# Optimization experiments

Hardware: AMD Instinct MI355X
Metric: run time of the kernel (lower is better)

The kernel has to match this reference:

```python
import jax, jax.numpy as jnp
import numpy as np

D_MODEL = 1024
N_HEADS = 16
D_HEAD = D_MODEL // N_HEADS
SCALE = 1.0 / (D_HEAD ** 0.5)


def _rel_shift(t):
    # Transformer-XL relative shift: pad -> view -> slice -> view. t: [b,h,q,k]
    b, h, q, k = t.shape
    padded = jnp.pad(t, ((0, 0), (0, 0), (0, 0), (1, 0)))  # [b,h,q,k+1]
    shifted = padded.reshape(b, h, k + 1, q)[:, :, 1:, :].reshape(b, h, q, k)
    return shifted


def setup_inputs() -> dict:
    key = jax.random.key(0)
    ks = jax.random.split(key, 10)
    B, T, M = 2, 1024, 1024
    J = M + T
    inp = {
        "x": jax.random.normal(ks[0], (B, T, D_MODEL), dtype=jnp.float32),
        "memory": jax.random.normal(ks[1], (B, M, D_MODEL), dtype=jnp.float32),
        "pos_emb": jax.random.normal(ks[2], (J, D_MODEL), dtype=jnp.float32),
        # nn.Linear(d, d, bias=False) weights: y = x @ W.T, W: [out, in]
        "q_w": jax.random.normal(ks[3], (D_MODEL, D_MODEL), dtype=jnp.float32) * 0.02,
        "k_w": jax.random.normal(ks[4], (D_MODEL, D_MODEL), dtype=jnp.float32) * 0.02,
        "v_w": jax.random.normal(ks[5], (D_MODEL, D_MODEL), dtype=jnp.float32) * 0.02,
        "r_w": jax.random.normal(ks[6], (D_MODEL, D_MODEL), dtype=jnp.float32) * 0.02,
        "out_w": jax.random.normal(ks[7], (D_MODEL, D_MODEL), dtype=jnp.float32) * 0.02,
        "pos_bias_u": jax.random.normal(ks[8], (N_HEADS, D_HEAD), dtype=jnp.float32) * 0.02,
        "pos_bias_v": jax.random.normal(ks[9], (N_HEADS, D_HEAD), dtype=jnp.float32) * 0.02,
    }
    return inp


def reference(x, memory, pos_emb, q_w, k_w, v_w, r_w, out_w, pos_bias_u, pos_bias_v):
    B, T, _ = x.shape
    cat = jnp.concatenate([memory, x], axis=1)  # [B, M+T, d]
    L = cat.shape[1]

    def heads(t):  # [B, time, d] -> [B, h, time, dh]
        return t.reshape(t.shape[0], t.shape[1], N_HEADS, D_HEAD).transpose(0, 2, 1, 3)

    q = heads(x @ q_w.T)      # [B,h,T,dh]
    k = heads(cat @ k_w.T)    # [B,h,L,dh]
    v = heads(cat @ v_w.T)    # [B,h,L,dh]
    r = (pos_emb @ r_w.T).reshape(-1, N_HEADS, D_HEAD).transpose(1, 0, 2)  # [h,J,dh]

    q_u = q + pos_bias_u[None, :, None, :]
    q_v = q + pos_bias_v[None, :, None, :]

    content_score = jnp.einsum('bhqd,bhkd->bhqk', q_u, k)  # [B,h,T,L]
    rel_score = jnp.einsum('bhqd,hjd->bhqj', q_v, r)        # [B,h,T,J]
    rel_score = _rel_shift(rel_score)

    scores = (content_score + rel_score) * SCALE
    attn = jax.nn.softmax(scores, axis=-1)
    out = jnp.einsum('bhqk,bhkd->bhqd', attn, v)            # [B,h,T,dh]
    out = out.transpose(0, 2, 1, 3).reshape(B, T, N_HEADS * D_HEAD)
    return out @ out_w.T
```

## Files before the change

kernel.cpp:

```cpp
#include <hip/hip_runtime.h>


typedef unsigned short u16;
typedef unsigned int u32;
typedef short bf16x8 __attribute__((ext_vector_type(8)));
typedef float f32x4 __attribute__((ext_vector_type(4)));

#define MFMA16(a, b, c) __builtin_amdgcn_mfma_f32_16x16x32_bf16(a, b, c, 0, 0, 0)

__device__ __forceinline__ u16 f2bf(float f) {
  u32 u = __float_as_uint(f);
  u32 r = (u + 0x7fffu + ((u >> 16) & 1u)) >> 16;
  return (u16)r;
}

__device__ __forceinline__ void async16(void* lds, const void* g) {
  __builtin_amdgcn_global_load_lds(
      (const __attribute__((address_space(1))) u32*)g,
      (__attribute__((address_space(3))) u32*)lds, 16, 0, 0);
}

__global__ void prep_kernel(const float* __restrict__ x, const float* __restrict__ mem,
                            const float* __restrict__ pos,
                            const float* __restrict__ qw, const float* __restrict__ kw,
                            const float* __restrict__ vw, const float* __restrict__ rw,
                            const float* __restrict__ ow,
                            u16* __restrict__ catb, u16* __restrict__ posb,
                            u16* __restrict__ wqb, u16* __restrict__ wkb,
                            u16* __restrict__ wvb, u16* __restrict__ wrb,
                            u16* __restrict__ wob) {
  const int seg = blockIdx.y;
  const int vid = blockIdx.x * blockDim.x + threadIdx.x;
  const float* src = nullptr;
  u16* dst = nullptr;
  int count = 0;
  switch (seg) {
    case 0: count = (2 * 2048 * 1024) / 4; dst = catb; break;
    case 1: count = (2048 * 1024) / 4; src = pos; dst = posb; break;
    case 2: count = (1024 * 1024) / 4; src = qw; dst = wqb; break;
    case 3: count = (1024 * 1024) / 4; src = kw; dst = wkb; break;
    case 4: count = (1024 * 1024) / 4; src = vw; dst = wvb; break;
    case 5: count = (1024 * 1024) / 4; src = rw; dst = wrb; break;
    case 6: count = (1024 * 1024) / 4; src = ow; dst = wob; break;
  }
  if (vid >= count) return;
  float4 f;
  if (seg == 0) {
    int e = vid * 4;
    int col = e & 1023;
    int row = (e >> 10) & 2047;
    int b = e >> 21;
    const float* s2 = (row < 1024)
                          ? (mem + ((size_t)(b * 1024 + row) * 1024 + col))
                          : (x + ((size_t)(b * 1024 + (row - 1024)) * 1024 + col));
    f = *(const float4*)s2;
  } else {
    f = *(const float4*)(src + (size_t)vid * 4);
  }
  ushort4 o4;
  o4.x = f2bf(f.x); o4.y = f2bf(f.y); o4.z = f2bf(f.z); o4.w = f2bf(f.w);
  *(ushort4*)(dst + (size_t)vid * 4) = o4;
}

__device__ __forceinline__ void gemm_core(const u16* __restrict__ A, const u16* __restrict__ W,
                                          u16* As, u16* Bs, int m0, int n0, bool qmap,
                                          f32x4 acc[4][4]) {
  const int t = threadIdx.x;
  const int lane = t & 63, wid = t >> 6;
  const int colL = lane & 15, rg = lane >> 4;
  const int wm = (wid >> 1) * 64, wn = (wid & 1) * 64;
  for (int kt = 0; kt < 32; ++kt) {
    __syncthreads();
#pragma unroll
    for (int pass = 0; pass < 2; ++pass) {
      int slot = t + pass * 256;
      int row = slot >> 2, ch = slot & 3;
      int sch = ch ^ ((row >> 1) & 3);
      int ar = m0 + row;
      if (qmap) ar = ((ar >> 10) << 11) + 1024 + (ar & 1023);
      async16(As + slot * 8, A + (size_t)ar * 1024 + kt * 32 + sch * 8);
      async16(Bs + slot * 8, W + (size_t)(n0 + row) * 1024 + kt * 32 + sch * 8);
    }
    __syncthreads();
    bf16x8 af[4], bfr[4];
#pragma unroll
    for (int mi = 0; mi < 4; ++mi) {
      int r = wm + mi * 16 + colL;
      af[mi] = *(const bf16x8*)(As + r * 32 + (rg ^ ((r >> 1) & 3)) * 8);
    }
#pragma unroll
    for (int ni = 0; ni < 4; ++ni) {
      int r = wn + ni * 16 + colL;
      bfr[ni] = *(const bf16x8*)(Bs + r * 32 + (rg ^ ((r >> 1) & 3)) * 8);
    }
#pragma unroll
    for (int mi = 0; mi < 4; ++mi)
#pragma unroll
      for (int ni = 0; ni < 4; ++ni)
        acc[mi][ni] = MFMA16(af[mi], bfr[ni], acc[mi][ni]);
  }
}

__global__ __launch_bounds__(256, 2) void gemm_qkvr(
    const u16* __restrict__ catb, const u16* __restrict__ posb,
    const u16* __restrict__ wqb, const u16* __restrict__ wrb,
    const u16* __restrict__ wkb, const u16* __restrict__ wvb,
    const float* __restrict__ bu, const float* __restrict__ bv,
    u16* __restrict__ qub, u16* __restrict__ qvb, u16* __restrict__ rbuf,
    u16* __restrict__ kbuf, u16* __restrict__ vtbuf) {
  __shared__ u16 As[128 * 32], Bs[128 * 32];
  const int x = blockIdx.x;
  const int bid = (x & 7) * 96 + (x >> 3);
  const u16* A;
  const u16* W;
  int mode, r2;
  bool qmap = false;
  if (bid < 128)      { mode = 0; A = catb; W = wqb; qmap = true; r2 = bid; }
  else if (bid < 256) { mode = 1; A = posb; W = wrb; r2 = bid - 128; }
  else if (bid < 512) { mode = 2; A = catb; W = wkb; r2 = bid - 256; }
  else                { mode = 3; A = catb; W = wvb; r2 = bid - 512; }
  const int m0 = (r2 >> 3) * 128, n0 = (r2 & 7) * 128;
  f32x4 acc[4][4];
  f32x4 zz = {0.f, 0.f, 0.f, 0.f};
#pragma unroll
  for (int a1 = 0; a1 < 4; ++a1)
#pragma unroll
    for (int a2 = 0; a2 < 4; ++a2) acc[a1][a2] = zz;
  gemm_core(A, W, As, Bs, m0, n0, qmap, acc);
  const int t = threadIdx.x, lane = t & 63, wid = t >> 6;
  const int colL = lane & 15, rg = lane >> 4;
  const int wm = (wid >> 1) * 64, wn = (wid & 1) * 64;
  const float sc = 0.18033688f;
#pragma unroll
  for (int mi = 0; mi < 4; ++mi)
#pragma unroll
    for (int ni = 0; ni < 4; ++ni)
#pragma unroll
      for (int e = 0; e < 4; ++e) {
        int m = m0 + wm + mi * 16 + rg * 4 + e;
        int n = n0 + wn + ni * 16 + colL;
        float val = acc[mi][ni][e];
        int hh = n >> 6, dd = n & 63;
        if (mode == 0) {
          int bb = m >> 10, tq = m & 1023;
          size_t ad = (((size_t)(bb * 16 + hh)) * 1024 + tq) * 64 + dd;
          qub[ad] = f2bf((val + bu[n]) * sc);
          qvb[ad] = f2bf((val + bv[n]) * sc);
        } else if (mode == 1) {
          rbuf[((((size_t)hh * 128 + (m >> 4)) * 8 + (dd >> 3)) * 16 + (m & 15)) * 8 +
               (dd & 7)] = f2bf(val);
        } else {
          int bb = m >> 11, j = m & 2047;
          size_t bh2 = (size_t)(bb * 16 + hh);
          if (mode == 2)
            kbuf[(((bh2 * 128 + (j >> 4)) * 8 + (dd >> 3)) * 16 + (j & 15)) * 8 + (dd & 7)] =
                f2bf(val);
          else
            vtbuf[((((bh2 * 32 + (j >> 6)) * 4 + (dd >> 4)) * 8 + ((j >> 3) & 7)) * 16 +
                   (dd & 15)) * 8 + (j & 7)] = f2bf(val);
        }
      }
}

__global__ __launch_bounds__(256, 2) void attn_kernel(
    const u16* __restrict__ qu, const u16* __restrict__ qv, const u16* __restrict__ ktile,
    const u16* __restrict__ vtile, const u16* __restrict__ rtile,
    float* __restrict__ opart, float* __restrict__ mlpart) {
  __shared__ float Ulds[4][3200];
  const int t = threadIdx.x;
  const int wid = t >> 6, lane = t & 63;
  const int colL = lane & 15, rg = lane >> 4;
  const int bid = ((blockIdx.x & 7) << 6) | (blockIdx.x >> 3);
  const int bh = bid >> 4;
  const int rem = bid & 15;
  const int qc = rem >> 1, ks = rem & 1;
  const int h = bh & 15;
  const int i0 = qc * 128 + wid * 32;

  const u16* qub = qu + (size_t)bh * (1024 * 64);
  const u16* qvb = qv + (size_t)bh * (1024 * 64);
  const u16* kb = ktile + (size_t)bh * (128 * 1024);
  const u16* vb = vtile + (size_t)bh * (32 * 4096);
  const u16* rb = rtile + (size_t)h * (128 * 1024);
  const int lane8 = (rg * 16 + colL) * 8;

  bf16x8 aqu0[2], aqv0[2], aqu1[2], aqv1[2];
  {
    int r0 = i0 + colL;
    int r1 = i0 + 16 + colL;
#pragma unroll
    for (int kx = 0; kx < 2; ++kx) {
      aqu0[kx] = *(const bf16x8*)(qub + (size_t)r0 * 64 + kx * 32 + rg * 8);
      aqv0[kx] = *(const bf16x8*)(qvb + (size_t)r0 * 64 + kx * 32 + rg * 8);
      aqu1[kx] = *(const bf16x8*)(qub + (size_t)r1 * 64 + kx * 32 + rg * 8);
      aqv1[kx] = *(const bf16x8*)(qvb + (size_t)r1 * 64 + kx * 32 + rg * 8);
    }
  }
  bf16x8 ones;
#pragma unroll
  for (int i = 0; i < 8; ++i) ones[i] = (short)0x3F80;

  const f32x4 zz = {0.f, 0.f, 0.f, 0.f};
  f32x4 o0[4], o1[4];
  f32x4 lacc0 = zz, lacc1 = zz;
#pragma unroll
  for (int e = 0; e < 4; ++e) { o0[e] = zz; o1[e] = zz; }
  int lb0[4], lb1[4];
#pragma unroll
  for (int e = 0; e < 4; ++e) {
    lb0[e] = (rg * 4 + e) * 99 + colL + 31;
    lb1[e] = (rg * 4 + e) * 99 + colL + 1615;
  }

  float* Uw = &Ulds[wid][0];
  u16* Pw = (u16*)Uw;

#pragma unroll 1
  for (int jt = ks * 16; jt < ks * 16 + 16; ++jt) {
    const int j0 = jt * 64;
    f32x4 s0[4], s1[4];
#pragma unroll
    for (int ni = 0; ni < 4; ++ni) {
      const u16* kp = kb + (size_t)((j0 >> 4) + ni) * 1024 + lane8;
      bf16x8 b0 = *(const bf16x8*)kp;
      bf16x8 b1 = *(const bf16x8*)(kp + 512);
      s0[ni] = zz;
      s0[ni] = MFMA16(aqu0[0], b0, s0[ni]);
      s0[ni] = MFMA16(aqu0[1], b1, s0[ni]);
      s1[ni] = zz;
      s1[ni] = MFMA16(aqu1[0], b0, s1[ni]);
      s1[ni] = MFMA16(aqu1[1], b1, s1[ni]);
    }
    const int pbase2 = j0 + 992 - i0;
    const bool mainv = (pbase2 <= 2047);
    const bool leak = (pbase2 + 94 >= 2049);
    if (mainv) {
      const int tb = pbase2 >> 4;
      bf16x8 rc[12];
#pragma unroll
      for (int uc = 0; uc < 6; ++uc) {
        int tt = tb + uc;
        tt = tt < 127 ? tt : 127;
        const u16* rp = rb + (size_t)tt * 1024 + lane8;
        rc[2 * uc] = *(const bf16x8*)rp;
        rc[2 * uc + 1] = *(const bf16x8*)(rp + 512);
      }
#pragma unroll
      for (int uc = 1; uc < 6; ++uc) {
        f32x4 ua = zz;
        ua = MFMA16(aqv0[0], rc[2 * uc], ua);
        ua = MFMA16(aqv0[1], rc[2 * uc + 1], ua);
#pragma unroll
        for (int e = 0; e < 4; ++e) Uw[(rg * 4 + e) * 100 + uc * 16 + colL] = ua[e];
      }
#pragma unroll
      for (int uc = 0; uc < 5; ++uc) {
        f32x4 ub = zz;
        ub = MFMA16(aqv1[0], rc[2 * uc], ub);
        ub = MFMA16(aqv1[1], rc[2 * uc + 1], ub);
#pragma unroll
        for (int e = 0; e < 4; ++e) Uw[(16 + rg * 4 + e) * 100 + uc * 16 + colL] = ub[e];
      }
      asm volatile("s_waitcnt lgkmcnt(0)" ::: "memory");
      const int pl0 = pbase2 + colL + 31;
      const int pl1 = pbase2 + colL + 15;
#pragma unroll
      for (int c = 0; c < 4; ++c)
#pragma unroll
        for (int e = 0; e < 4; ++e) {
          int w0e = rg * 4 + e;
          float u0 = Uw[lb0[e] + c * 16];
          float u1 = Uw[lb1[e] + c * 16];
          int p0 = pl0 + c * 16 - w0e;
          int p1 = pl1 + c * 16 - w0e;
          s0[c][e] += (p0 <= 2047) ? u0 : 0.f;
          s1[c][e] += (p1 <= 2047) ? u1 : 0.f;
        }
    }
    if (leak) {
      asm volatile("s_waitcnt lgkmcnt(0)" ::: "memory");
      bf16x8 aqs0[2], aqs1[2];
      {
        int rs0 = i0 + colL + 1;
        int rs1 = i0 + 16 + colL + 1;
        rs1 = rs1 < 1024 ? rs1 : 1023;
#pragma unroll
        for (int kx = 0; kx < 2; ++kx) {
          aqs0[kx] = *(const bf16x8*)(qvb + (size_t)rs0 * 64 + kx * 32 + rg * 8);
          aqs1[kx] = *(const bf16x8*)(qvb + (size_t)rs1 * 64 + kx * 32 + rg * 8);
        }
      }
      const int mB1 = (pbase2 - 2048) >> 4;
      const int rowL = (colL + 15) & 15;
      const int tadj = (colL > 0) ? 0 : -1;
      bf16x8 r2[12];
#pragma unroll
      for (int uc = 0; uc < 6; ++uc) {
        int tL = mB1 + uc + tadj;
        tL = tL < 0 ? 0 : (tL > 127 ? 127 : tL);
        const u16* rp = rb + (size_t)tL * 1024 + rg * 128 + rowL * 8;
        r2[2 * uc] = *(const bf16x8*)rp;
        r2[2 * uc + 1] = *(const bf16x8*)(rp + 512);
      }
#pragma unroll
      for (int uc = 1; uc < 6; ++uc) {
        f32x4 ua = zz;
        ua = MFMA16(aqs0[0], r2[2 * uc], ua);
        ua = MFMA16(aqs0[1], r2[2 * uc + 1], ua);
#pragma unroll
        for (int e = 0; e < 4; ++e) Uw[(rg * 4 + e) * 100 + uc * 16 + colL] = ua[e];
      }
#pragma unroll
      for (int uc = 0; uc < 5; ++uc) {
        f32x4 ub = zz;
        ub = MFMA16(aqs1[0], r2[2 * uc], ub);
        ub = MFMA16(aqs1[1], r2[2 * uc + 1], ub);
#pragma unroll
        for (int e = 0; e < 4; ++e) Uw[(16 + rg * 4 + e) * 100 + uc * 16 + colL] = ub[e];
      }
      asm volatile("s_waitcnt lgkmcnt(0)" ::: "memory");
      const int pl0 = pbase2 + colL + 31;
      const int pl1 = pbase2 + colL + 15;
#pragma unroll
      for (int c = 0; c < 4; ++c)
#pragma unroll
        for (int e = 0; e < 4; ++e) {
          int w0e = rg * 4 + e;
          int p0 = pl0 + c * 16 - w0e;
          int p1 = pl1 + c * 16 - w0e;
          if (p0 >= 2049) s0[c][e] += Uw[lb0[e] + c * 16];
          if (p1 >= 2049) s1[c][e] += Uw[lb1[e] + c * 16];
        }
    }
    bf16x8 vf[8];
    {
      const u16* vp0 = vb + (size_t)jt * 4096 + lane8;
#pragma unroll
      for (int ni = 0; ni < 4; ++ni) {
        vf[2 * ni] = *(const bf16x8*)(vp0 + ni * 1024);
        vf[2 * ni + 1] = *(const bf16x8*)(vp0 + ni * 1024 + 512);
      }
    }
#pragma unroll
    for (int c = 0; c < 4; ++c)
#pragma unroll
      for (int e = 0; e < 4; ++e) {
        int row = rg * 4 + e;
        int col = c * 16 + colL;
        int sw = (col >> 3) ^ (row & 7);
        float p0 = __builtin_amdgcn_exp2f(s0[c][e] - 16.0f);
        float p1 = __builtin_amdgcn_exp2f(s1[c][e] - 16.0f);
        Pw[row * 64 + sw * 8 + (colL & 7)] = f2bf(p0);
        Pw[(16 + row) * 64 + sw * 8 + (colL & 7)] = f2bf(p1);
      }
    asm volatile("s_waitcnt lgkmcnt(0)" ::: "memory");
    bf16x8 pa0[2], pa1[2];
#pragma unroll
    for (int kx = 0; kx < 2; ++kx) {
      int chunk = kx * 4 + rg;
      int sw = chunk ^ (colL & 7);
      pa0[kx] = *(const bf16x8*)(Pw + colL * 64 + sw * 8);
      pa1[kx] = *(const bf16x8*)(Pw + (16 + colL) * 64 + sw * 8);
    }
    lacc0 = MFMA16(pa0[0], ones, lacc0);
    lacc0 = MFMA16(pa0[1], ones, lacc0);
    lacc1 = MFMA16(pa1[0], ones, lacc1);
    lacc1 = MFMA16(pa1[1], ones, lacc1);
#pragma unroll
    for (int ni = 0; ni < 4; ++ni) {
      o0[ni] = MFMA16(pa0[0], vf[2 * ni], o0[ni]);
      o0[ni] = MFMA16(pa0[1], vf[2 * ni + 1], o0[ni]);
      o1[ni] = MFMA16(pa1[0], vf[2 * ni], o1[ni]);
      o1[ni] = MFMA16(pa1[1], vf[2 * ni + 1], o1[ni]);
    }
    asm volatile("" ::: "memory");
  }
  const size_t rowbase = (size_t)ks * 32768 + (size_t)bh * 1024 + i0;
#pragma unroll
  for (int c = 0; c < 4; ++c)
#pragma unroll
    for (int e = 0; e < 4; ++e) {
      int row = rg * 4 + e;
      opart[(rowbase + row) * 64 + c * 16 + colL] = o0[c][e];
      opart[(rowbase + 16 + row) * 64 + c * 16 + colL] = o1[c][e];
    }
  if (colL == 0) {
#pragma unroll
    for (int e = 0; e < 4; ++e) {
      size_t r = rowbase + rg * 4 + e;
      mlpart[r * 2 + 0] = 16.0f;
      mlpart[r * 2 + 1] = lacc0[e];
      mlpart[(r + 16) * 2 + 0] = 16.0f;
      mlpart[(r + 16) * 2 + 1] = lacc1[e];
    }
  }
}

__global__ void combine_kernel(const float* __restrict__ opart,
                               const float* __restrict__ mlpart,
                               u16* __restrict__ aout) {
  const int gid = blockIdx.x * 256 + threadIdx.x;
  const int r = gid >> 4;
  const int cg = gid & 15;
  float2 ml0 = *(const float2*)(mlpart + (size_t)r * 2);
  float2 ml1 = *(const float2*)(mlpart + ((size_t)32768 + r) * 2);
  float m = fmaxf(ml0.x, ml1.x);
  float f0 = __builtin_amdgcn_exp2f(ml0.x - m);
  float f1 = __builtin_amdgcn_exp2f(ml1.x - m);
  float inv = 1.0f / (ml0.y * f0 + ml1.y * f1);
  f0 *= inv; f1 *= inv;
  float4 a = *(const float4*)(opart + (size_t)r * 64 + cg * 4);
  float4 b4 = *(const float4*)(opart + ((size_t)32768 + r) * 64 + cg * 4);
  ushort4 o4;
  o4.x = f2bf(a.x * f0 + b4.x * f1);
  o4.y = f2bf(a.y * f0 + b4.y * f1);
  o4.z = f2bf(a.z * f0 + b4.z * f1);
  o4.w = f2bf(a.w * f0 + b4.w * f1);
  const int bh = r >> 10, i = r & 1023;
  const int b = bh >> 4, h = bh & 15;
  *(ushort4*)(aout + ((size_t)(b * 1024 + i) * 1024 + h * 64 + cg * 4)) = o4;
}

__global__ __launch_bounds__(256, 2) void gemm_out(
    const u16* __restrict__ aob, const u16* __restrict__ wob, float* __restrict__ out) {
  __shared__ u16 As[128 * 32], Bs[128 * 32];
  const int bid = ((blockIdx.x & 7) << 4) | (blockIdx.x >> 3);
  const int mt = bid >> 3, nt = bid & 7;
  const int m0 = mt * 128, n0 = nt * 128;
  f32x4 acc[4][4];
  f32x4 zz = {0.f, 0.f, 0.f, 0.f};
#pragma unroll
  for (int a1 = 0; a1 < 4; ++a1)
#pragma unroll
    for (int a2 = 0; a2 < 4; ++a2) acc[a1][a2] = zz;
  gemm_core(aob, wob, As, Bs, m0, n0, false, acc);
  const int t = threadIdx.x, lane = t & 63, wid = t >> 6;
  const int colL = lane & 15, rg = lane >> 4;
  const int wm = (wid >> 1) * 64, wn = (wid & 1) * 64;
#pragma unroll
  for (int mi = 0; mi < 4; ++mi)
#pragma unroll
    for (int ni = 0; ni < 4; ++ni)
#pragma unroll
      for (int e = 0; e < 4; ++e) {
        int m = m0 + wm + mi * 16 + rg * 4 + e;
        int n = n0 + wn + ni * 16 + colL;
        out[(size_t)m * 1024 + n] = acc[mi][ni][e];
      }
}

extern "C" void kernel_launch(void* const* d_in, const int* in_sizes, int n_in,
                              void* d_out, int out_size, void* d_ws, size_t ws_size,
                              hipStream_t stream) {
  (void)in_sizes; (void)n_in; (void)out_size; (void)ws_size;
  const float* x = (const float*)d_in[0];
  const float* mem = (const float*)d_in[1];
  const float* pos = (const float*)d_in[2];
  const float* qw = (const float*)d_in[3];
  const float* kw = (const float*)d_in[4];
  const float* vw = (const float*)d_in[5];
  const float* rw = (const float*)d_in[6];
  const float* ow = (const float*)d_in[7];
  const float* bu = (const float*)d_in[8];
  const float* bv = (const float*)d_in[9];
  float* out = (float*)d_out;

  char* w = (char*)d_ws;
  u16* catb = (u16*)(w + 0);
  u16* posb = (u16*)(w + 8388608);
  u16* wqb  = (u16*)(w + 12582912);
  u16* wkb  = (u16*)(w + 14680064);
  u16* wvb  = (u16*)(w + 16777216);
  u16* wrb  = (u16*)(w + 18874368);
  u16* wob  = (u16*)(w + 20971520);
  u16* qub  = (u16*)(w + 23068672);
  u16* qvb  = (u16*)(w + 27262976);
  u16* kbuf = (u16*)(w + 31457280);
  u16* vtb  = (u16*)(w + 39845888);
  u16* rbuf = (u16*)(w + 48234496);
  u16* aob  = (u16*)(w + 52428800);
  float* opart  = (float*)(w + 0);
  float* mlpart = (float*)(w + 16777216);

  prep_kernel<<<dim3(4096, 7), 256, 0, stream>>>(x, mem, pos, qw, kw, vw, rw, ow,
                                                 catb, posb, wqb, wkb, wvb, wrb, wob);
  gemm_qkvr<<<768, 256, 0, stream>>>(catb, posb, wqb, wrb, wkb, wvb, bu, bv,
                                     qub, qvb, rbuf, kbuf, vtb);
  attn_kernel<<<512, 256, 0, stream>>>(qub, qvb, kbuf, vtb, rbuf, opart, mlpart);
  combine_kernel<<<2048, 256, 0, stream>>>(opart, mlpart, aob);
  gemm_out<<<128, 256, 0, stream>>>(aob, wob, out);
}
```

Measured before the change: 226.2 us.

## Transpose V epilogue through LDS for vector stores; raise priority around MFMA blocks

The V projection epilogue used to scatter single bf16 values into the tiled transposed V buffer. It now packs each accumulator fragment to bf16 in a per-wave LDS tile, transposes there, and writes 16-byte vectors to global memory, aiming to cut uncoalesced narrow stores. The attention kernel also wraps its MFMA clusters in s_setprio so waves issuing matrix work get scheduling priority over waves doing loads or softmax. This adds LDS use to the GEMM kernel, which could affect occupancy, and the priority hints may not help.

```diff
diff --git a/kernel.cpp b/kernel.cpp
--- a/kernel.cpp
+++ b/kernel.cpp
@@ -109,6 +109,7 @@
     u16* __restrict__ qub, u16* __restrict__ qvb, u16* __restrict__ rbuf,
     u16* __restrict__ kbuf, u16* __restrict__ vtbuf) {
   __shared__ u16 As[128 * 32], Bs[128 * 32];
+  __shared__ u16 Ep[4][16 * 72];
   const int x = blockIdx.x;
   const int bid = (x & 7) * 96 + (x >> 3);
   const u16* A;
@@ -131,6 +132,35 @@
   const int colL = lane & 15, rg = lane >> 4;
   const int wm = (wid >> 1) * 64, wn = (wid & 1) * 64;
   const float sc = 0.18033688f;
+  if (mode == 3) {
+    u16* Ew = &Ep[wid][0];
+    const int bb = m0 >> 11;
+    const int j0w = (m0 + wm) & 2047;
+    const int hh = (n0 + wn) >> 6;
+    const size_t vb0 =
+        (((size_t)(bb * 16 + hh) * 32 + (j0w >> 6)) * 4) * 1024;
+#pragma unroll
+    for (int ni = 0; ni < 4; ++ni) {
+#pragma unroll
+      for (int mi = 0; mi < 4; ++mi) {
+        u32 lo = (u32)f2bf(acc[mi][ni][0]) | ((u32)f2bf(acc[mi][ni][1]) << 16);
+        u32 hi = (u32)f2bf(acc[mi][ni][2]) | ((u32)f2bf(acc[mi][ni][3]) << 16);
+        uint2 pk; pk.x = lo; pk.y = hi;
+        *(uint2*)(Ew + colL * 72 + mi * 16 + rg * 4) = pk;
+      }
+      asm volatile("s_waitcnt lgkmcnt(0)" ::: "memory");
+      const size_t vb = vb0 + (size_t)ni * 1024;
+#pragma unroll
+      for (int rr = 0; rr < 2; ++rr) {
+        int ch = rr * 4 + rg;
+        int dr = colL;
+        bf16x8 vv = *(const bf16x8*)(Ew + dr * 72 + ch * 8);
+        *(bf16x8*)(vtbuf + vb + ch * 128 + dr * 8) = vv;
+      }
+      asm volatile("s_waitcnt lgkmcnt(0)" ::: "memory");
+    }
+    return;
+  }
 #pragma unroll
   for (int mi = 0; mi < 4; ++mi)
 #pragma unroll
@@ -152,12 +182,8 @@
         } else {
           int bb = m >> 11, j = m & 2047;
           size_t bh2 = (size_t)(bb * 16 + hh);
-          if (mode == 2)
-            kbuf[(((bh2 * 128 + (j >> 4)) * 8 + (dd >> 3)) * 16 + (j & 15)) * 8 + (dd & 7)] =
-                f2bf(val);
-          else
-            vtbuf[((((bh2 * 32 + (j >> 6)) * 4 + (dd >> 4)) * 8 + ((j >> 3) & 7)) * 16 +
-                   (dd & 15)) * 8 + (j & 7)] = f2bf(val);
+          kbuf[(((bh2 * 128 + (j >> 4)) * 8 + (dd >> 3)) * 16 + (j & 15)) * 8 + (dd & 7)] =
+              f2bf(val);
         }
       }
 }
@@ -219,6 +245,7 @@
   for (int jt = ks * 16; jt < ks * 16 + 16; ++jt) {
     const int j0 = jt * 64;
     f32x4 s0[4], s1[4];
+    __builtin_amdgcn_s_setprio(1);
 #pragma unroll
     for (int ni = 0; ni < 4; ++ni) {
       const u16* kp = kb + (size_t)((j0 >> 4) + ni) * 1024 + lane8;
@@ -231,6 +258,7 @@
       s1[ni] = MFMA16(aqu1[0], b0, s1[ni]);
       s1[ni] = MFMA16(aqu1[1], b1, s1[ni]);
     }
+    __builtin_amdgcn_s_setprio(0);
     const int pbase2 = j0 + 992 - i0;
     const bool mainv = (pbase2 <= 2047);
     const bool leak = (pbase2 + 94 >= 2049);
@@ -245,6 +273,7 @@
         rc[2 * uc] = *(const bf16x8*)rp;
         rc[2 * uc + 1] = *(const bf16x8*)(rp + 512);
       }
+      __builtin_amdgcn_s_setprio(1);
 #pragma unroll
       for (int uc = 1; uc < 6; ++uc) {
         f32x4 ua = zz;
@@ -261,6 +290,7 @@
 #pragma unroll
         for (int e = 0; e < 4; ++e) Uw[(16 + rg * 4 + e) * 100 + uc * 16 + colL] = ub[e];
       }
+      __builtin_amdgcn_s_setprio(0);
       asm volatile("s_waitcnt lgkmcnt(0)" ::: "memory");
       const int pl0 = pbase2 + colL + 31;
       const int pl1 = pbase2 + colL + 15;
@@ -302,6 +332,7 @@
         r2[2 * uc] = *(const bf16x8*)rp;
         r2[2 * uc + 1] = *(const bf16x8*)(rp + 512);
       }
+      __builtin_amdgcn_s_setprio(1);
 #pragma unroll
       for (int uc = 1; uc < 6; ++uc) {
         f32x4 ua = zz;
@@ -318,6 +349,7 @@
 #pragma unroll
         for (int e = 0; e < 4; ++e) Uw[(16 + rg * 4 + e) * 100 + uc * 16 + colL] = ub[e];
       }
+      __builtin_amdgcn_s_setprio(0);
       asm volatile("s_waitcnt lgkmcnt(0)" ::: "memory");
       const int pl0 = pbase2 + colL + 31;
       const int pl1 = pbase2 + colL + 15;
@@ -362,6 +394,7 @@
       pa0[kx] = *(const bf16x8*)(Pw + colL * 64 + sw * 8);
       pa1[kx] = *(const bf16x8*)(Pw + (16 + colL) * 64 + sw * 8);
     }
+    __builtin_amdgcn_s_setprio(1);
     lacc0 = MFMA16(pa0[0], ones, lacc0);
     lacc0 = MFMA16(pa0[1], ones, lacc0);
     lacc1 = MFMA16(pa1[0], ones, lacc1);
@@ -373,6 +406,7 @@
       o1[ni] = MFMA16(pa1[0], vf[2 * ni], o1[ni]);
       o1[ni] = MFMA16(pa1[1], vf[2 * ni + 1], o1[ni]);
     }
+    __builtin_amdgcn_s_setprio(0);
     asm volatile("" ::: "memory");
   }
   const size_t rowbase = (size_t)ks * 32768 + (size_t)bh * 1024 + i0;
```

Result: no change. 227.5 us (+0.6%).
